# Kernel optimization log

Measured on AMD Instinct MI355X. Metric: run time of the kernel, lower is better.

## Reference

```python
import jax, jax.numpy as jnp
import numpy as np

NUM_CLASSES = 1024   # encoder feature dim; conv1 in_channels = NUM_CLASSES + 5 = 1029
GRID = 4             # grid_size
NUM_COARSE = 1024    # hard-coded in module
GG = GRID * GRID
NUM_FINE = GG * NUM_COARSE  # 16384
BATCH = 8


def _init(key, shape, fan_in):
    return (jax.random.normal(key, shape, jnp.float32) / np.sqrt(fan_in)).astype(jnp.float32)


def setup_inputs() -> dict:
    key = jax.random.key(0)
    ks = jax.random.split(key, 7)
    fea = jax.random.normal(ks[0], (BATCH, NUM_CLASSES), jnp.float32)
    # linear1: num_classes -> 1024 ; linear2: 1024 -> num_coarse*3
    W_l1 = _init(ks[1], (NUM_CLASSES, 1024), NUM_CLASSES)
    b_l1 = jnp.zeros((1024,), jnp.float32)
    W_l2 = _init(ks[2], (1024, NUM_COARSE * 3), 1024)
    b_l2 = jnp.zeros((NUM_COARSE * 3,), jnp.float32)
    # 1x1 convs act as per-point linears over the channel dim
    W_c1 = _init(ks[3], (NUM_CLASSES + 5, 512), NUM_CLASSES + 5)
    b_c1 = jnp.zeros((512,), jnp.float32)
    W_c2 = _init(ks[4], (512, 512), 512)
    b_c2 = jnp.zeros((512,), jnp.float32)
    W_c3 = _init(ks[5], (512, 3), 512)
    b_c3 = jnp.zeros((3,), jnp.float32)
    return {
        "fea": fea,
        "W_l1": W_l1, "b_l1": b_l1, "W_l2": W_l2, "b_l2": b_l2,
        "W_c1": W_c1, "b_c1": b_c1, "W_c2": W_c2, "b_c2": b_c2,
        "W_c3": W_c3, "b_c3": b_c3,
    }


def reference(fea, W_l1, b_l1, W_l2, b_l2, W_c1, b_c1, W_c2, b_c2, W_c3, b_c3):
    B = fea.shape[0]
    # coarse point prediction: (B, NUM_COARSE, 3)
    x = jax.nn.relu(fea @ W_l1 + b_l1) @ W_l2 + b_l2
    x = x.reshape(B, NUM_COARSE, 3)

    # 2D folding grid: grid[i*GRID + j] = (d[j], d[i])  (matches torch repeat/t())
    d = jnp.linspace(-0.05, 0.05, GRID, dtype=jnp.float32)
    gx, gy = jnp.meshgrid(d, d)            # 'xy': gx[i,j]=d[j], gy[i,j]=d[i]
    grid = jnp.stack([gx, gy], axis=-1).reshape(GG, 2)

    # grid tiled over coarse points: (B, NUM_FINE, 2)
    grid_feat = jnp.tile(grid[None], (B, NUM_COARSE, 1))
    # each coarse point repeated GG consecutive times: (B, NUM_FINE, 3)
    point_feat = jnp.repeat(x, GG, axis=1)
    # global feature broadcast to all fine points: (B, NUM_FINE, NUM_CLASSES)
    global_feat = jnp.broadcast_to(fea[:, None, :], (B, NUM_FINE, NUM_CLASSES))

    feat = jnp.concatenate([grid_feat, point_feat, global_feat], axis=2)  # (B, NUM_FINE, 1029)

    # 1x1 conv stack == pointwise MLP over channels
    h = jax.nn.relu(feat @ W_c1 + b_c1)
    h = jax.nn.relu(h @ W_c2 + b_c2)
    fine = h @ W_c3 + b_c3 + point_feat   # center == point_feat
    return (x, fine)
```

## Files before the change

kernel.cpp:

```cpp
#include <hip/hip_runtime.h>
#include <hip/hip_bf16.h>
#include <stdint.h>

typedef __hip_bfloat16 bf16;
typedef __attribute__((ext_vector_type(8))) short v8s;
typedef __attribute__((ext_vector_type(4))) float v4f;

__device__ __forceinline__ bf16 tob(float x) { return __float2bfloat16(x); }

__device__ __forceinline__ void gload16(const void* g, void* l) {
  __builtin_amdgcn_global_load_lds(
      (const __attribute__((address_space(1))) uint32_t*)g,
      (__attribute__((address_space(3))) uint32_t*)l,
      16, 0, 0);
}

__device__ __forceinline__ float red16(float v) {
  v += __int_as_float(__builtin_amdgcn_update_dpp(0, __float_as_int(v), 0xB1, 0xF, 0xF, true));
  v += __int_as_float(__builtin_amdgcn_update_dpp(0, __float_as_int(v), 0x4E, 0xF, 0xF, true));
  v += __int_as_float(__builtin_amdgcn_update_dpp(0, __float_as_int(v), 0x141, 0xF, 0xF, true));
  v += __int_as_float(__builtin_amdgcn_update_dpp(0, __float_as_int(v), 0x140, 0xF, 0xF, true));
  return v;
}

__global__ void k_pre(const float* __restrict__ fea, const float* __restrict__ Wl1,
                      const float* __restrict__ bl1, const float* __restrict__ Wc1,
                      const float* __restrict__ bc1, const float* __restrict__ Wc2,
                      float* __restrict__ h1, float* __restrict__ gp,
                      bf16* __restrict__ WT, float* __restrict__ G,
                      float* __restrict__ fine) {
  __shared__ __align__(16) float sm[32 * 33 + 32];
  const int bid = blockIdx.x;
  if (bid < 512) {
    float* red = sm;
    const int nl = threadIdx.x & 15, ks = threadIdx.x >> 4;
    const int o = bid * 16 + nl;
    const int b = o >> 10, n = o & 1023;
    const float* fr = fea + (b << 10) + ks * 64;
    const float* wp = Wl1 + (size_t)(ks * 64) * 1024 + n;
    float acc = 0.f;
#pragma unroll 8
    for (int j = 0; j < 64; ++j)
      acc = fmaf(fr[j], wp[(size_t)j * 1024], acc);
    red[threadIdx.x] = acc;
    __syncthreads();
    if (threadIdx.x < 16) {
      float s = bl1[n];
#pragma unroll
      for (int i = 0; i < 16; ++i) s += red[i * 16 + threadIdx.x];
      h1[o] = fmaxf(s, 0.f);
    }
  } else if (bid < 768) {
    float* red = sm;
    const int nl = threadIdx.x & 15, ks = threadIdx.x >> 4;
    const int o = (bid - 512) * 16 + nl;
    const int b = o >> 9, n = o & 511;
    const float* fr = fea + (b << 10) + ks * 64;
    const float* wp = Wc1 + (size_t)(5 + ks * 64) * 512 + n;
    float acc = 0.f;
#pragma unroll 8
    for (int j = 0; j < 64; ++j)
      acc = fmaf(fr[j], wp[(size_t)j * 512], acc);
    red[threadIdx.x] = acc;
    __syncthreads();
    if (threadIdx.x < 16) {
      float s = bc1[n];
#pragma unroll
      for (int i = 0; i < 16; ++i) s += red[i * 16 + threadIdx.x];
      gp[o] = s;
    }
  } else if (bid < 1024) {
    float (*tile)[33] = (float(*)[33])sm;
    const int bb = bid - 768;
    int bx = bb & 15, by = bb >> 4;
    int c = threadIdx.x & 31, r8 = threadIdx.x >> 5;
#pragma unroll
    for (int i = 0; i < 4; ++i) {
      int r = r8 + i * 8;
      tile[r][c] = Wc2[(by * 32 + r) * 512 + bx * 32 + c];
    }
    __syncthreads();
#pragma unroll
    for (int i = 0; i < 4; ++i) {
      int r = r8 + i * 8;
      int n = bx * 32 + r;
      int k = by * 32 + c;
      int s = (c >> 3) & 3;
      int ks = (k & ~24) | (((s ^ ((n >> 1) & 3)) & 3) << 3);
      WT[(size_t)n * 512 + ks] = tob(tile[c][r]);
    }
  } else if (bid == 1024) {
    for (int e = threadIdx.x; e < 8192; e += 256) {
      int g = e >> 9, k = e & 511;
      const float gx = -0.05f + (float)(g & 3) * (0.1f / 3.0f);
      const float gy = -0.05f + (float)(g >> 2) * (0.1f / 3.0f);
      G[e] = fmaf(gy, Wc1[512 + k], gx * Wc1[k]);
    }
  } else {
    const int i = ((bid - 1025) * 256 + threadIdx.x) * 4;
    *(float4*)(fine + i) = (float4){0.f, 0.f, 0.f, 0.f};
  }
}

__global__ void k_lin2(const float* __restrict__ h1, const float* __restrict__ W,
                       const float* __restrict__ bias, float* __restrict__ xf,
                       float* __restrict__ xout) {
  __shared__ float h1s[8][1024];
  __shared__ float red[16][16][9];
  const int t = threadIdx.x;
  const int n0 = blockIdx.x * 16;
  for (int i = t; i < 8192; i += 256)
    ((float*)h1s)[i] = h1[i];
  __syncthreads();
  const int nl = t & 15, ks = t >> 4;
  const int n = n0 + nl;
  float acc[8] = {0.f, 0.f, 0.f, 0.f, 0.f, 0.f, 0.f, 0.f};
  const float* wp = W + (size_t)(ks * 64) * 3072 + n;
#pragma unroll 8
  for (int j = 0; j < 64; ++j) {
    float wv = wp[(size_t)j * 3072];
    const float* hk = &h1s[0][ks * 64 + j];
#pragma unroll
    for (int b = 0; b < 8; ++b) acc[b] = fmaf(hk[b * 1024], wv, acc[b]);
  }
#pragma unroll
  for (int b = 0; b < 8; ++b) red[ks][nl][b] = acc[b];
  __syncthreads();
  if (t < 128) {
    const int nn = t & 15, b = t >> 4;
    float s = bias[n0 + nn];
#pragma unroll
    for (int i = 0; i < 16; ++i) s += red[i][nn][b];
    const int o = b * 3072 + n0 + nn;
    xf[o] = s;
    xout[o] = s;
  }
}

__global__ __launch_bounds__(512, 4)
void k_gemm(const bf16* __restrict__ W2T, const float* __restrict__ gp,
            const float* __restrict__ G, const float* __restrict__ Wc1,
            const float* __restrict__ xf, const float* __restrict__ bc2,
            const float* __restrict__ Wc3, const float* __restrict__ bc3,
            float* __restrict__ fine) {
  __shared__ __align__(16) bf16 As[2][128 * 32];
  __shared__ __align__(16) bf16 Bs[2][256 * 32];
  __shared__ __align__(16) float Ps[8][512];
  __shared__ float facc4[4][128][3];
  const int t = threadIdx.x;
  const int mblk = blockIdx.x >> 1, nblk = blockIdx.x & 1;
  const int m0 = mblk * 128;
  const int w = t >> 6, l = t & 63, q = l >> 4, lm = l & 15;
  const int wm = (w >> 2) * 64;
  const int wn = (w & 3) * 64;
  const int qs = (q ^ ((lm >> 1) & 3)) << 4;

  const int arow = t >> 2, cg = t & 3;
  const int m = m0 + arow;
  const int b = m >> 14;
  const int f = m & 16383;
  const int g = f & 15;
  const float* gr = G + (g << 9);
  const float* pl = Ps[arow >> 4];
  char* awr = (char*)As + arow * 64 + ((cg ^ ((arow >> 1) & 3)) << 4);

  {
    const int cl = t >> 6;
    const int k8 = (t & 63) * 8;
    const int cglob = ((m0 & 16383) >> 4) + cl;
    const float* xq = xf + (b * 1024 + cglob) * 3;
    const float x0 = xq[0], x1 = xq[1], x2 = xq[2];
    const float* gpb = gp + (b << 9) + k8;
    float4 gv0 = *(const float4*)(gpb);
    float4 gv1 = *(const float4*)(gpb + 4);
    float4 w20 = *(const float4*)(Wc1 + 2 * 512 + k8);
    float4 w21 = *(const float4*)(Wc1 + 2 * 512 + k8 + 4);
    float4 w30 = *(const float4*)(Wc1 + 3 * 512 + k8);
    float4 w31 = *(const float4*)(Wc1 + 3 * 512 + k8 + 4);
    float4 w40 = *(const float4*)(Wc1 + 4 * 512 + k8);
    float4 w41 = *(const float4*)(Wc1 + 4 * 512 + k8 + 4);
    float4 r0, r1;
#pragma unroll
    for (int j = 0; j < 4; ++j) {
      ((float*)&r0)[j] = fmaf(x2, ((const float*)&w40)[j],
                         fmaf(x1, ((const float*)&w30)[j],
                         fmaf(x0, ((const float*)&w20)[j], ((const float*)&gv0)[j])));
      ((float*)&r1)[j] = fmaf(x2, ((const float*)&w41)[j],
                         fmaf(x1, ((const float*)&w31)[j],
                         fmaf(x0, ((const float*)&w21)[j], ((const float*)&gv1)[j])));
    }
    *(float4*)&Ps[cl][k8] = r0;
    *(float4*)&Ps[cl][k8 + 4] = r1;
  }

  const char* bsrc = (const char*)W2T +
      (size_t)(nblk * 256 + w * 32 + (l >> 2)) * 1024 + (l & 3) * 16;
  char* bdst = (char*)Bs + w * 2048 + l * 16;

  v4f acc[4][4];
#pragma unroll
  for (int mi = 0; mi < 4; ++mi)
#pragma unroll
    for (int ni = 0; ni < 4; ++ni) acc[mi][ni] = (v4f){0.f, 0.f, 0.f, 0.f};

  float4 ga0, ga1;
  auto loadG = [&](int kt) {
    const int kk = kt * 32 + cg * 8;
    ga0 = *(const float4*)(gr + kk);
    ga1 = *(const float4*)(gr + kk + 4);
  };
  auto stage = [&](int kt, int buf) {
    const char* src = bsrc + kt * 64;
    char* dst = bdst + buf * 16384;
    gload16(src, dst);
    gload16(src + 16384, dst + 1024);
    const int kk = kt * 32 + cg * 8;
    float4 p0 = *(const float4*)(pl + kk);
    float4 p1 = *(const float4*)(pl + kk + 4);
    union { bf16 h[8]; uint4 u; } o;
#pragma unroll
    for (int j = 0; j < 4; ++j) {
      o.h[j]     = tob(fmaxf(((const float*)&p0)[j] + ((const float*)&ga0)[j], 0.f));
      o.h[4 + j] = tob(fmaxf(((const float*)&p1)[j] + ((const float*)&ga1)[j], 0.f));
    }
    *(uint4*)(awr + buf * 8192) = o.u;
  };

  loadG(0);
  __syncthreads();
  stage(0, 0);
  loadG(1);

#pragma unroll 2
  for (int kt = 0; kt < 16; ++kt) {
    const int buf = kt & 1;
    __syncthreads();
    if (kt < 15) {
      stage(kt + 1, buf ^ 1);
      if (kt < 14) loadG(kt + 2);
    }
    const char* ab = (const char*)As + buf * 8192;
    const char* bb = (const char*)Bs + buf * 16384;
    v8s af[4], bfr[4];
#pragma unroll
    for (int mi = 0; mi < 4; ++mi)
      af[mi] = *(const v8s*)(ab + (wm + mi * 16 + lm) * 64 + qs);
#pragma unroll
    for (int ni = 0; ni < 4; ++ni)
      bfr[ni] = *(const v8s*)(bb + (wn + ni * 16 + lm) * 64 + qs);
#pragma unroll
    for (int mi = 0; mi < 4; ++mi)
#pragma unroll
      for (int ni = 0; ni < 4; ++ni)
        acc[mi][ni] = __builtin_amdgcn_mfma_f32_16x16x32_bf16(af[mi], bfr[ni], acc[mi][ni], 0, 0, 0);
  }

  float part[4][4][3];
#pragma unroll
  for (int mi = 0; mi < 4; ++mi)
#pragma unroll
    for (int r = 0; r < 4; ++r) { part[mi][r][0] = 0.f; part[mi][r][1] = 0.f; part[mi][r][2] = 0.f; }
#pragma unroll
  for (int ni = 0; ni < 4; ++ni) {
    const int n = nblk * 256 + wn + ni * 16 + lm;
    const float bv = bc2[n];
    const float w30 = Wc3[n * 3 + 0];
    const float w31 = Wc3[n * 3 + 1];
    const float w32 = Wc3[n * 3 + 2];
#pragma unroll
    for (int mi = 0; mi < 4; ++mi)
#pragma unroll
      for (int r = 0; r < 4; ++r) {
        float v = fmaxf(acc[mi][ni][r] + bv, 0.f);
        part[mi][r][0] = fmaf(v, w30, part[mi][r][0]);
        part[mi][r][1] = fmaf(v, w31, part[mi][r][1]);
        part[mi][r][2] = fmaf(v, w32, part[mi][r][2]);
      }
  }
#pragma unroll
  for (int mi = 0; mi < 4; ++mi)
#pragma unroll
    for (int r = 0; r < 4; ++r)
#pragma unroll
      for (int j = 0; j < 3; ++j) {
        float v = red16(part[mi][r][j]);
        if (lm == 0) facc4[w & 3][wm + mi * 16 + q * 4 + r][j] = v;
      }
  __syncthreads();
  if (t < 128) {
    const int mm = m0 + t;
    float* fp = fine + (size_t)mm * 3;
    float base[3] = {0.f, 0.f, 0.f};
    if (nblk == 0) {
      const int bb2 = mm >> 14, cc = (mm & 16383) >> 4;
      const float* xq = xf + (bb2 * 1024 + cc) * 3;
#pragma unroll
      for (int j = 0; j < 3; ++j) base[j] = bc3[j] + xq[j];
    }
#pragma unroll
    for (int j = 0; j < 3; ++j) {
      float s = facc4[0][t][j] + facc4[1][t][j] + facc4[2][t][j] + facc4[3][t][j];
      atomicAdd(&fp[j], s + base[j]);
    }
  }
}

extern "C" void kernel_launch(void* const* d_in, const int* in_sizes, int n_in,
                              void* d_out, int out_size, void* d_ws, size_t ws_size,
                              hipStream_t stream) {
  const float* fea = (const float*)d_in[0];
  const float* Wl1 = (const float*)d_in[1];
  const float* bl1 = (const float*)d_in[2];
  const float* Wl2 = (const float*)d_in[3];
  const float* bl2 = (const float*)d_in[4];
  const float* Wc1 = (const float*)d_in[5];
  const float* bc1 = (const float*)d_in[6];
  const float* Wc2 = (const float*)d_in[7];
  const float* bc2 = (const float*)d_in[8];
  const float* Wc3 = (const float*)d_in[9];
  const float* bc3 = (const float*)d_in[10];
  float* xout = (float*)d_out;
  float* fine = (float*)d_out + 24576;
  char* ws = (char*)d_ws;
  float* h1  = (float*)ws;
  float* xf  = (float*)(ws + 32768);
  float* gp  = (float*)(ws + 131072);
  bf16*  W2T = (bf16*)(ws + 147456);
  float* G   = (float*)(ws + 671744);

  k_pre<<<1409, 256, 0, stream>>>(fea, Wl1, bl1, Wc1, bc1, Wc2, h1, gp, W2T, G, fine);
  k_lin2<<<192, 256, 0, stream>>>(h1, Wl2, bl2, xf, xout);
  k_gemm<<<2048, 512, 0, stream>>>(W2T, gp, G, Wc1, xf, bc2, Wc3, bc3, fine);
}
```

Measured before the change: 173.5 us.

## Build A-operand fragments directly in registers instead of staging through LDS

The first-layer activation tile (relu of the per-coarse-point projection plus the grid term) is now computed per wave straight into MFMA A fragments. It reads the shared per-point rows and the grid rows for each 16-row subtile, rather than writing bf16 tiles to an LDS buffer and reading them back. This removes the As shared buffer, its writes and reads, and part of the barrier traffic. In exchange every wave recomputes the relu/convert work for its fragments, which duplicates that work across the N-direction waves. It also reads fp32 Ps from LDS with more bytes per fragment.

```diff
diff --git a/kernel.cpp b/kernel.cpp
--- a/kernel.cpp
+++ b/kernel.cpp
@@ -143,7 +143,6 @@
             const float* __restrict__ xf, const float* __restrict__ bc2,
             const float* __restrict__ Wc3, const float* __restrict__ bc3,
             float* __restrict__ fine) {
-  __shared__ __align__(16) bf16 As[2][128 * 32];
   __shared__ __align__(16) bf16 Bs[2][256 * 32];
   __shared__ __align__(16) float Ps[8][512];
   __shared__ float facc4[4][128][3];
@@ -154,15 +153,7 @@
   const int wm = (w >> 2) * 64;
   const int wn = (w & 3) * 64;
   const int qs = (q ^ ((lm >> 1) & 3)) << 4;
-
-  const int arow = t >> 2, cg = t & 3;
-  const int m = m0 + arow;
-  const int b = m >> 14;
-  const int f = m & 16383;
-  const int g = f & 15;
-  const float* gr = G + (g << 9);
-  const float* pl = Ps[arow >> 4];
-  char* awr = (char*)As + arow * 64 + ((cg ^ ((arow >> 1) & 3)) << 4);
+  const int b = m0 >> 14;
 
   {
     const int cl = t >> 6;
@@ -197,6 +188,9 @@
       (size_t)(nblk * 256 + w * 32 + (l >> 2)) * 1024 + (l & 3) * 16;
   char* bdst = (char*)Bs + w * 2048 + l * 16;
 
+  const float* grow = G + (lm << 9);
+  const float* pbase = Ps[(w >> 2) * 4];
+
   v4f acc[4][4];
 #pragma unroll
   for (int mi = 0; mi < 4; ++mi)
@@ -205,54 +199,48 @@
 
   float4 ga0, ga1;
   auto loadG = [&](int kt) {
-    const int kk = kt * 32 + cg * 8;
-    ga0 = *(const float4*)(gr + kk);
-    ga1 = *(const float4*)(gr + kk + 4);
+    const int kk = kt * 32 + q * 8;
+    ga0 = *(const float4*)(grow + kk);
+    ga1 = *(const float4*)(grow + kk + 4);
   };
   auto stage = [&](int kt, int buf) {
     const char* src = bsrc + kt * 64;
     char* dst = bdst + buf * 16384;
     gload16(src, dst);
     gload16(src + 16384, dst + 1024);
-    const int kk = kt * 32 + cg * 8;
-    float4 p0 = *(const float4*)(pl + kk);
-    float4 p1 = *(const float4*)(pl + kk + 4);
-    union { bf16 h[8]; uint4 u; } o;
-#pragma unroll
-    for (int j = 0; j < 4; ++j) {
-      o.h[j]     = tob(fmaxf(((const float*)&p0)[j] + ((const float*)&ga0)[j], 0.f));
-      o.h[4 + j] = tob(fmaxf(((const float*)&p1)[j] + ((const float*)&ga1)[j], 0.f));
-    }
-    *(uint4*)(awr + buf * 8192) = o.u;
   };
 
   loadG(0);
   __syncthreads();
   stage(0, 0);
-  loadG(1);
 
 #pragma unroll 2
   for (int kt = 0; kt < 16; ++kt) {
     const int buf = kt & 1;
     __syncthreads();
-    if (kt < 15) {
-      stage(kt + 1, buf ^ 1);
-      if (kt < 14) loadG(kt + 2);
-    }
-    const char* ab = (const char*)As + buf * 8192;
+    if (kt < 15) stage(kt + 1, buf ^ 1);
     const char* bb = (const char*)Bs + buf * 16384;
-    v8s af[4], bfr[4];
-#pragma unroll
-    for (int mi = 0; mi < 4; ++mi)
-      af[mi] = *(const v8s*)(ab + (wm + mi * 16 + lm) * 64 + qs);
+    v8s bfr[4];
 #pragma unroll
     for (int ni = 0; ni < 4; ++ni)
       bfr[ni] = *(const v8s*)(bb + (wn + ni * 16 + lm) * 64 + qs);
-#pragma unroll
-    for (int mi = 0; mi < 4; ++mi)
+    const int kk = kt * 32 + q * 8;
+#pragma unroll
+    for (int mi = 0; mi < 4; ++mi) {
+      const float* pr = pbase + mi * 512 + kk;
+      float4 p0 = *(const float4*)(pr);
+      float4 p1 = *(const float4*)(pr + 4);
+      union { bf16 h[8]; v8s v; } af;
+#pragma unroll
+      for (int j = 0; j < 4; ++j) {
+        af.h[j]     = tob(fmaxf(((const float*)&p0)[j] + ((const float*)&ga0)[j], 0.f));
+        af.h[4 + j] = tob(fmaxf(((const float*)&p1)[j] + ((const float*)&ga1)[j], 0.f));
+      }
 #pragma unroll
       for (int ni = 0; ni < 4; ++ni)
-        acc[mi][ni] = __builtin_amdgcn_mfma_f32_16x16x32_bf16(af[mi], bfr[ni], acc[mi][ni], 0, 0, 0);
+        acc[mi][ni] = __builtin_amdgcn_mfma_f32_16x16x32_bf16(af.v, bfr[ni], acc[mi][ni], 0, 0, 0);
+    }
+    if (kt < 15) loadG(kt + 1);
   }
 
   float part[4][4][3];
```

After: 204.2 us. +17.6%, slower.
